# Performance work log

Hardware: AMD Instinct MI355X
Metric: run time of the kernel (lower is better)

The kernel has to match this reference:

```python
import jax, jax.numpy as jnp
import numpy as np

STATE_MASS = 4.0
EPS = 1e-5
LOW_RANK_SCALE = 0.1  # _LOW_RANK_SCALE_INIT


def _ln(x, g, b):
    mu = jnp.mean(x, axis=-1, keepdims=True)
    var = jnp.var(x, axis=-1, keepdims=True)
    return (x - mu) * jax.lax.rsqrt(var + EPS) * g + b


def _signed_abs_softmax(s, axis=-1):
    s = jnp.nan_to_num(s)
    return jnp.sign(s) * jax.nn.softmax(jnp.abs(s), axis=axis)


def _signed_softmax_state(st):
    st = jnp.nan_to_num(st)
    return jnp.sign(st) * jax.nn.softmax(jnp.abs(st), axis=-1) * STATE_MASS


def _low_rank_scores(dst, src, Ut_w, Ut_b, Us_w, Us_b, w):
    # bilinear low-rank pairwise: score[b,i,j] = sum_r (dst_i Ut)_r * w_r * (src_j Us)_r
    pt = dst @ Ut_w + Ut_b                      # [B,Nd,R]
    ps = src @ Us_w + Us_b                      # [B,Ns,R]
    return jnp.einsum('bir,r,bjr->bij', pt, w * LOW_RANK_SCALE, ps)


def _gather_rows(x, idx):
    # x: [B,N,...], idx: [B,M,K] -> [B,M,K,...] (per-batch gather, no NxM broadcast)
    return jax.vmap(lambda xi, ii: xi[ii])(x, idx)


def setup_inputs() -> dict:
    key = jax.random.key(0)
    ks = jax.random.split(key, 8)
    B, S, D, M, R = 16, 2048, 512, 256, 64
    std = 0.02
    return {
        'token_val': jax.random.normal(ks[0], (B, S, D), jnp.float32),
        'token_state': jax.random.normal(ks[1], (B, S), jnp.float32),
        'init_state': jax.random.normal(ks[2], (M,), jnp.float32) * std,
        'init_val': jax.random.normal(ks[3], (M, D), jnp.float32) * std,
        'rUs_w': jax.random.normal(ks[4], (D, R), jnp.float32) * std,
        'rUs_b': jnp.zeros((R,), jnp.float32),
        'rUt_w': jax.random.normal(ks[5], (D, R), jnp.float32) * std,
        'rUt_b': jnp.zeros((R,), jnp.float32),
        'r_w': jnp.ones((R,), jnp.float32),
        'pUs_w': jax.random.normal(ks[6], (D, R), jnp.float32) * std,
        'pUs_b': jnp.zeros((R,), jnp.float32),
        'pUt_w': jax.random.normal(ks[7], (D, R), jnp.float32) * std,
        'pUt_b': jnp.zeros((R,), jnp.float32),
        'p_w': jnp.ones((R,), jnp.float32),
        'ln_g': jnp.ones((D,), jnp.float32),
        'ln_b': jnp.zeros((D,), jnp.float32),
        'topk': 16,
    }


def reference(token_val, token_state, init_state, init_val,
              rUs_w, rUs_b, rUt_w, rUt_b, r_w,
              pUs_w, pUs_b, pUt_w, pUt_b, p_w,
              ln_g, ln_b, topk):
    B = token_val.shape[0]
    M, D = init_val.shape

    # _MemoryLevel.initialize
    mem_state = _signed_softmax_state(jnp.broadcast_to(init_state, (B, M)))
    mem_val = _ln(jnp.broadcast_to(init_val, (B, M, D)), ln_g, ln_b)

    # ---- SparseTransition (write): route tokens -> slots, top-k sources/slot ----
    scores = _low_rank_scores(mem_val, token_val, rUt_w, rUt_b, rUs_w, rUs_b, r_w)  # [B,M,S]
    _, idx = jax.lax.top_k(jnp.abs(scores), topk)              # [B,M,K]
    sel = jnp.take_along_axis(scores, idx, axis=-1)            # [B,M,K]
    edges = _signed_abs_softmax(sel, axis=-1)                  # signed-abs-softmax over edges
    v_sel = _gather_rows(token_val, idx)                       # [B,M,K,D]
    s_sel = _gather_rows(token_state, idx)                     # [B,M,K]
    mem_val = mem_val + jnp.einsum('bmk,bmkd->bmd', edges, v_sel)   # merge_mode='add'
    mem_state = mem_state + jnp.einsum('bmk,bmk->bm', edges, s_sel)
    mem_state = _signed_softmax_state(mem_state)
    mem_val = _ln(mem_val, ln_g, ln_b)

    # ---- SparsePropagation within slots: state-weighted top-k edges, residual ----
    pscores = _low_rank_scores(mem_val, mem_val, pUt_w, pUt_b, pUs_w, pUs_b, p_w)   # [B,M,M]
    pscores = pscores * mem_state[:, None, :]                  # state_weight_edges
    _, pidx = jax.lax.top_k(jnp.abs(pscores), topk)            # [B,M,K]
    psel = jnp.take_along_axis(pscores, pidx, axis=-1)
    pe = _signed_abs_softmax(psel, axis=-1)
    pv = _gather_rows(mem_val, pidx)                           # [B,M,K,D]
    pst = _gather_rows(mem_state, pidx)                        # [B,M,K]
    mem_val = mem_val + jnp.einsum('bmk,bmkd->bmd', pe, pv)    # residual=True
    mem_state = mem_state + jnp.einsum('bmk,bmk->bm', pe, pst)
    mem_state = _signed_softmax_state(mem_state)
    mem_val = _ln(mem_val, ln_g, ln_b)
    return mem_val
```

## Files before the change

### kernel.cpp

```cpp
#include <hip/hip_runtime.h>
#include <hip/hip_bf16.h>
#include <math.h>

#define BB 16
#define SS 2048
#define DD 512
#define MM 256
#define RR 64
#define KK 16
#define GPAD 68

__device__ __forceinline__ float wave_sum(float v) {
#pragma unroll
  for (int off = 32; off > 0; off >>= 1) v += __shfl_xor(v, off);
  return v;
}

__device__ __forceinline__ float sgnf(float v) {
  return (v > 0.f) ? 1.f : ((v < 0.f) ? -1.f : 0.f);
}

__global__ __launch_bounds__(256) void k_init(
    const float* __restrict__ init_val, const float* __restrict__ ln_g,
    const float* __restrict__ ln_b, const float* __restrict__ rUt_w,
    const float* __restrict__ rUt_b, const float* __restrict__ r_w,
    float* __restrict__ mv0, float* __restrict__ pt0) {
  int m = blockIdx.x, t = threadIdx.x;
  __shared__ float row[DD];
  __shared__ float red[8];
  float x0 = init_val[m * DD + t];
  float x1 = init_val[m * DD + t + 256];
  float s = wave_sum(x0 + x1);
  float sq = wave_sum(x0 * x0 + x1 * x1);
  if ((t & 63) == 0) { red[t >> 6] = s; red[4 + (t >> 6)] = sq; }
  __syncthreads();
  float mean = (red[0] + red[1] + red[2] + red[3]) * (1.0f / DD);
  float var = (red[4] + red[5] + red[6] + red[7]) * (1.0f / DD) - mean * mean;
  float rs = rsqrtf(var + 1e-5f);
  float n0 = (x0 - mean) * rs * ln_g[t] + ln_b[t];
  float n1 = (x1 - mean) * rs * ln_g[t + 256] + ln_b[t + 256];
  mv0[m * DD + t] = n0;
  mv0[m * DD + t + 256] = n1;
  row[t] = n0;
  row[t + 256] = n1;
  __syncthreads();
  if (t < RR) {
    float acc = rUt_b[t];
    for (int d = 0; d < DD; ++d) acc += row[d] * rUt_w[d * RR + t];
    pt0[m * RR + t] = acc * r_w[t] * 0.1f;
  }
}

__global__ __launch_bounds__(256) void k_state_softmax(
    const float* __restrict__ in, float* __restrict__ out) {
  int b = blockIdx.x, t = threadIdx.x;
  __shared__ float red[4];
  float v = in[b * MM + t];
  float a = fabsf(v);
  float mx = a;
#pragma unroll
  for (int off = 32; off > 0; off >>= 1) mx = fmaxf(mx, __shfl_xor(mx, off));
  if ((t & 63) == 0) red[t >> 6] = mx;
  __syncthreads();
  mx = fmaxf(fmaxf(red[0], red[1]), fmaxf(red[2], red[3]));
  __syncthreads();
  float e = expf(a - mx);
  float ssum = wave_sum(e);
  if ((t & 63) == 0) red[t >> 6] = ssum;
  __syncthreads();
  ssum = red[0] + red[1] + red[2] + red[3];
  out[b * MM + t] = sgnf(v) * e / ssum * 4.0f;
}

__global__ __launch_bounds__(256) void k_ps(
    const float* __restrict__ A, const float* __restrict__ W,
    const float* __restrict__ bias, float* __restrict__ C0,
    float* __restrict__ C1) {
  __shared__ float Ast[32][128];
  __shared__ float Ws[32][RR];
  int t = threadIdx.x;
  int lane = t & 63;
  int wv = t >> 6;
  int tx = t & 15;
  int ty = t >> 4;
  int half = blockIdx.x >> 8;
  int row0 = (blockIdx.x & 255) * 128;
  int k0 = half * 256;
  float* C = half ? C1 : C0;
  float4 ra[4];
  float4 rw[2];
#pragma unroll
  for (int i = 0; i < 4; ++i) {
    int r = (i & 1) * 64 + lane;
    int k4 = (i >> 1) * 4 + wv;
    ra[i] = *reinterpret_cast<const float4*>(
        &A[(size_t)(row0 + r) * DD + k0 + k4 * 4]);
  }
#pragma unroll
  for (int i = 0; i < 2; ++i) {
    int slot = i * 256 + t;
    int k = slot >> 4, c4 = slot & 15;
    rw[i] = *reinterpret_cast<const float4*>(&W[(size_t)(k0 + k) * RR + c4 * 4]);
  }
  float acc[8][4] = {};
  for (int c = 0; c < 8; ++c) {
    __syncthreads();
#pragma unroll
    for (int i = 0; i < 4; ++i) {
      int r = (i & 1) * 64 + lane;
      int k4 = (i >> 1) * 4 + wv;
      Ast[k4 * 4 + 0][r] = ra[i].x;
      Ast[k4 * 4 + 1][r] = ra[i].y;
      Ast[k4 * 4 + 2][r] = ra[i].z;
      Ast[k4 * 4 + 3][r] = ra[i].w;
    }
#pragma unroll
    for (int i = 0; i < 2; ++i) {
      int slot = i * 256 + t;
      int k = slot >> 4, c4 = slot & 15;
      *reinterpret_cast<float4*>(&Ws[k][c4 * 4]) = rw[i];
    }
    __syncthreads();
    if (c < 7) {
      int kc = k0 + (c + 1) * 32;
#pragma unroll
      for (int i = 0; i < 4; ++i) {
        int r = (i & 1) * 64 + lane;
        int k4 = (i >> 1) * 4 + wv;
        ra[i] = *reinterpret_cast<const float4*>(
            &A[(size_t)(row0 + r) * DD + kc + k4 * 4]);
      }
#pragma unroll
      for (int i = 0; i < 2; ++i) {
        int slot = i * 256 + t;
        int k = slot >> 4, c4 = slot & 15;
        rw[i] = *reinterpret_cast<const float4*>(
            &W[(size_t)(kc + k) * RR + c4 * 4]);
      }
    }
#pragma unroll
    for (int k = 0; k < 32; ++k) {
      float4 alo = *reinterpret_cast<const float4*>(&Ast[k][ty * 8]);
      float4 ahi = *reinterpret_cast<const float4*>(&Ast[k][ty * 8 + 4]);
      float4 w4 = *reinterpret_cast<const float4*>(&Ws[k][tx * 4]);
      acc[0][0] += alo.x * w4.x; acc[0][1] += alo.x * w4.y; acc[0][2] += alo.x * w4.z; acc[0][3] += alo.x * w4.w;
      acc[1][0] += alo.y * w4.x; acc[1][1] += alo.y * w4.y; acc[1][2] += alo.y * w4.z; acc[1][3] += alo.y * w4.w;
      acc[2][0] += alo.z * w4.x; acc[2][1] += alo.z * w4.y; acc[2][2] += alo.z * w4.z; acc[2][3] += alo.z * w4.w;
      acc[3][0] += alo.w * w4.x; acc[3][1] += alo.w * w4.y; acc[3][2] += alo.w * w4.z; acc[3][3] += alo.w * w4.w;
      acc[4][0] += ahi.x * w4.x; acc[4][1] += ahi.x * w4.y; acc[4][2] += ahi.x * w4.z; acc[4][3] += ahi.x * w4.w;
      acc[5][0] += ahi.y * w4.x; acc[5][1] += ahi.y * w4.y; acc[5][2] += ahi.y * w4.z; acc[5][3] += ahi.y * w4.w;
      acc[6][0] += ahi.z * w4.x; acc[6][1] += ahi.z * w4.y; acc[6][2] += ahi.z * w4.z; acc[6][3] += ahi.z * w4.w;
      acc[7][0] += ahi.w * w4.x; acc[7][1] += ahi.w * w4.y; acc[7][2] += ahi.w * w4.z; acc[7][3] += ahi.w * w4.w;
    }
  }
  float4 bv;
  if (half == 0) {
    bv = *reinterpret_cast<const float4*>(&bias[tx * 4]);
  } else {
    bv.x = bv.y = bv.z = bv.w = 0.f;
  }
#pragma unroll
  for (int r = 0; r < 8; ++r) {
    int rr = row0 + ty * 8 + r;
    float4 o;
    o.x = acc[r][0] + bv.x; o.y = acc[r][1] + bv.y;
    o.z = acc[r][2] + bv.z; o.w = acc[r][3] + bv.w;
    *reinterpret_cast<float4*>(&C[(size_t)rr * RR + tx * 4]) = o;
  }
}

template <bool TRANS_OUT>
__device__ __forceinline__ void gemm_body(
    const float* __restrict__ A, const float* __restrict__ W,
    const float* __restrict__ bias, const float* __restrict__ colscale,
    float csmul, const float* __restrict__ rowscale, float* __restrict__ C,
    int row0, float (*Ast)[GPAD], float (*Ws)[GPAD]) {
  int tid = threadIdx.x;
  int ty = tid >> 4, tx = tid & 15;
  float acc[4][4] = {};
  for (int kc = 0; kc < DD; kc += 32) {
#pragma unroll
    for (int i = 0; i < 2; ++i) {
      int s4 = i * 256 + tid;
      int r = s4 >> 3;
      int k4 = s4 & 7;
      float4 v = *reinterpret_cast<const float4*>(
          &A[(size_t)(row0 + r) * DD + kc + k4 * 4]);
      Ast[k4 * 4 + 0][r] = v.x;
      Ast[k4 * 4 + 1][r] = v.y;
      Ast[k4 * 4 + 2][r] = v.z;
      Ast[k4 * 4 + 3][r] = v.w;
    }
#pragma unroll
    for (int i = 0; i < 2; ++i) {
      int s4 = i * 256 + tid;
      int r = s4 >> 4;
      int c4 = s4 & 15;
      float4 v = *reinterpret_cast<const float4*>(
          &W[(size_t)(kc + r) * RR + c4 * 4]);
      *reinterpret_cast<float4*>(&Ws[r][c4 * 4]) = v;
    }
    __syncthreads();
#pragma unroll
    for (int k = 0; k < 32; ++k) {
      float4 a4 = *reinterpret_cast<const float4*>(&Ast[k][ty * 4]);
      float4 w4 = *reinterpret_cast<const float4*>(&Ws[k][tx * 4]);
      acc[0][0] += a4.x * w4.x; acc[0][1] += a4.x * w4.y;
      acc[0][2] += a4.x * w4.z; acc[0][3] += a4.x * w4.w;
      acc[1][0] += a4.y * w4.x; acc[1][1] += a4.y * w4.y;
      acc[1][2] += a4.y * w4.z; acc[1][3] += a4.y * w4.w;
      acc[2][0] += a4.z * w4.x; acc[2][1] += a4.z * w4.y;
      acc[2][2] += a4.z * w4.z; acc[2][3] += a4.z * w4.w;
      acc[3][0] += a4.w * w4.x; acc[3][1] += a4.w * w4.y;
      acc[3][2] += a4.w * w4.z; acc[3][3] += a4.w * w4.w;
    }
    __syncthreads();
  }
#pragma unroll
  for (int i = 0; i < 4; ++i) {
    int rr = row0 + ty * 4 + i;
    float rsc = rowscale ? rowscale[rr] : 1.f;
#pragma unroll
    for (int j = 0; j < 4; ++j) {
      int cc = tx * 4 + j;
      float v = acc[i][j] + bias[cc];
      if (colscale) v *= colscale[cc] * csmul;
      v *= rsc;
      if (TRANS_OUT) {
        C[((size_t)(rr >> 8) * RR + cc) * MM + (rr & 255)] = v;
      } else {
        C[(size_t)rr * RR + cc] = v;
      }
    }
  }
}

__global__ __launch_bounds__(256) void k_gemm_pair(
    const float* __restrict__ mv1, const float* __restrict__ pUt_w,
    const float* __restrict__ pUt_b, const float* __restrict__ p_w,
    const float* __restrict__ pUs_w, const float* __restrict__ pUs_b,
    const float* __restrict__ ms1, float* __restrict__ pt1,
    float* __restrict__ ps1T) {
  __shared__ float Ast[32][GPAD];
  __shared__ float Ws[32][GPAD];
  if (blockIdx.x < 64) {
    gemm_body<false>(mv1, pUt_w, pUt_b, p_w, 0.1f, nullptr, pt1,
                     blockIdx.x * 64, Ast, Ws);
  } else {
    gemm_body<true>(mv1, pUs_w, pUs_b, nullptr, 1.f, ms1, ps1T,
                    (blockIdx.x - 64) * 64, Ast, Ws);
  }
}

#define PSW 144
__device__ __forceinline__ int psw(int j) { return j + ((j >> 5) << 2); }

__global__ __launch_bounds__(256) void k_scores(
    const float* __restrict__ pt0, const float* __restrict__ ps0,
    const float* __restrict__ ps1, float* __restrict__ scores) {
  __shared__ float PtT[RR][64];
  __shared__ float PsT[RR][PSW];
  int t = threadIdx.x;
  int b = blockIdx.z;
  int m0 = blockIdx.y * 64;
  int j0 = blockIdx.x * 128;
  {
    int tm4 = t >> 4, tk4 = t & 15;
    const float* base = pt0 + (size_t)(m0 + tm4 * 4) * RR + tk4 * 4;
    float4 v0 = *reinterpret_cast<const float4*>(base);
    float4 v1 = *reinterpret_cast<const float4*>(base + RR);
    float4 v2 = *reinterpret_cast<const float4*>(base + 2 * RR);
    float4 v3 = *reinterpret_cast<const float4*>(base + 3 * RR);
    float4 w;
    w.x = v0.x; w.y = v1.x; w.z = v2.x; w.w = v3.x;
    *reinterpret_cast<float4*>(&PtT[tk4 * 4 + 0][tm4 * 4]) = w;
    w.x = v0.y; w.y = v1.y; w.z = v2.y; w.w = v3.y;
    *reinterpret_cast<float4*>(&PtT[tk4 * 4 + 1][tm4 * 4]) = w;
    w.x = v0.z; w.y = v1.z; w.z = v2.z; w.w = v3.z;
    *reinterpret_cast<float4*>(&PtT[tk4 * 4 + 2][tm4 * 4]) = w;
    w.x = v0.w; w.y = v1.w; w.z = v2.w; w.w = v3.w;
    *reinterpret_cast<float4*>(&PtT[tk4 * 4 + 3][tm4 * 4]) = w;
  }
#pragma unroll
  for (int ii = 0; ii < 2; ++ii) {
    int slot = ii * 256 + t;
    int jt = slot >> 4, kt = slot & 15;
    size_t off = ((size_t)b * SS + j0 + jt * 4) * RR + kt * 4;
    const float* base0 = ps0 + off;
    const float* base1 = ps1 + off;
    float4 v0 = *reinterpret_cast<const float4*>(base0);
    float4 v1 = *reinterpret_cast<const float4*>(base0 + RR);
    float4 v2 = *reinterpret_cast<const float4*>(base0 + 2 * RR);
    float4 v3 = *reinterpret_cast<const float4*>(base0 + 3 * RR);
    float4 u0 = *reinterpret_cast<const float4*>(base1);
    float4 u1 = *reinterpret_cast<const float4*>(base1 + RR);
    float4 u2 = *reinterpret_cast<const float4*>(base1 + 2 * RR);
    float4 u3 = *reinterpret_cast<const float4*>(base1 + 3 * RR);
    v0.x += u0.x; v0.y += u0.y; v0.z += u0.z; v0.w += u0.w;
    v1.x += u1.x; v1.y += u1.y; v1.z += u1.z; v1.w += u1.w;
    v2.x += u2.x; v2.y += u2.y; v2.z += u2.z; v2.w += u2.w;
    v3.x += u3.x; v3.y += u3.y; v3.z += u3.z; v3.w += u3.w;
    int jc = psw(jt * 4);
    float4 w;
    w.x = v0.x; w.y = v1.x; w.z = v2.x; w.w = v3.x;
    *reinterpret_cast<float4*>(&PsT[kt * 4 + 0][jc]) = w;
    w.x = v0.y; w.y = v1.y; w.z = v2.y; w.w = v3.y;
    *reinterpret_cast<float4*>(&PsT[kt * 4 + 1][jc]) = w;
    w.x = v0.z; w.y = v1.z; w.z = v2.z; w.w = v3.z;
    *reinterpret_cast<float4*>(&PsT[kt * 4 + 2][jc]) = w;
    w.x = v0.w; w.y = v1.w; w.z = v2.w; w.w = v3.w;
    *reinterpret_cast<float4*>(&PsT[kt * 4 + 3][jc]) = w;
  }
  __syncthreads();
  int tj = t & 15;
  int tm = t >> 4;
  int jlo = psw(tj * 8);
  int jhi = psw(tj * 8 + 4);
  float acc[4][8] = {};
#pragma unroll
  for (int k = 0; k < RR; ++k) {
    float4 a4 = *reinterpret_cast<const float4*>(&PtT[k][tm * 4]);
    float4 w0 = *reinterpret_cast<const float4*>(&PsT[k][jlo]);
    float4 w1 = *reinterpret_cast<const float4*>(&PsT[k][jhi]);
    acc[0][0] += a4.x * w0.x; acc[0][1] += a4.x * w0.y; acc[0][2] += a4.x * w0.z; acc[0][3] += a4.x * w0.w;
    acc[0][4] += a4.x * w1.x; acc[0][5] += a4.x * w1.y; acc[0][6] += a4.x * w1.z; acc[0][7] += a4.x * w1.w;
    acc[1][0] += a4.y * w0.x; acc[1][1] += a4.y * w0.y; acc[1][2] += a4.y * w0.z; acc[1][3] += a4.y * w0.w;
    acc[1][4] += a4.y * w1.x; acc[1][5] += a4.y * w1.y; acc[1][6] += a4.y * w1.z; acc[1][7] += a4.y * w1.w;
    acc[2][0] += a4.z * w0.x; acc[2][1] += a4.z * w0.y; acc[2][2] += a4.z * w0.z; acc[2][3] += a4.z * w0.w;
    acc[2][4] += a4.z * w1.x; acc[2][5] += a4.z * w1.y; acc[2][6] += a4.z * w1.z; acc[2][7] += a4.z * w1.w;
    acc[3][0] += a4.w * w0.x; acc[3][1] += a4.w * w0.y; acc[3][2] += a4.w * w0.z; acc[3][3] += a4.w * w0.w;
    acc[3][4] += a4.w * w1.x; acc[3][5] += a4.w * w1.y; acc[3][6] += a4.w * w1.z; acc[3][7] += a4.w * w1.w;
  }
  float* obase = scores + (size_t)b * MM * SS + (size_t)(m0 + tm * 4) * SS + j0 + tj * 8;
#pragma unroll
  for (int i = 0; i < 4; ++i) {
    float4 o0, o1;
    o0.x = acc[i][0]; o0.y = acc[i][1]; o0.z = acc[i][2]; o0.w = acc[i][3];
    o1.x = acc[i][4]; o1.y = acc[i][5]; o1.z = acc[i][6]; o1.w = acc[i][7];
    *reinterpret_cast<float4*>(obase + (size_t)i * SS) = o0;
    *reinterpret_cast<float4*>(obase + (size_t)i * SS + 4) = o1;
  }
}

__global__ __launch_bounds__(256) void k_write(
    const float* __restrict__ scores, const float* __restrict__ token_val,
    const float* __restrict__ token_state, const float* __restrict__ mv0,
    const float* __restrict__ ms0, const float* __restrict__ ln_g,
    const float* __restrict__ ln_b, float* __restrict__ mv1,
    float* __restrict__ ms_w) {
  int t = threadIdx.x;
  int wave = t >> 6, lane = t & 63;
  int i = blockIdx.x;
  int slot = i >> 3;
  int b = 2 * (i & 7) + (slot >> 6);
  int m = (slot & 63) * 4 + wave;
  int row = b * MM + m;
  __shared__ float srl[4][SS];
  __shared__ int selj_sh[4][KK];
  float4* srl4 = reinterpret_cast<float4*>(&srl[wave][0]);
  const float* srow = scores + (size_t)row * SS;
  unsigned maxa = 0u;
#pragma unroll
  for (int ch = 0; ch < 8; ++ch) {
    float4 q = *reinterpret_cast<const float4*>(srow + (ch * 64 + lane) * 4);
    srl4[ch * 64 + lane] = q;
    maxa = max(maxa, __float_as_uint(q.x) & 0x7fffffffu);
    maxa = max(maxa, __float_as_uint(q.y) & 0x7fffffffu);
    maxa = max(maxa, __float_as_uint(q.z) & 0x7fffffffu);
    maxa = max(maxa, __float_as_uint(q.w) & 0x7fffffffu);
  }
#pragma unroll
  for (int off = 32; off > 0; off >>= 1)
    maxa = max(maxa, (unsigned)__shfl_xor((int)maxa, off));
  unsigned lo = 0u, hi = maxa, thr = 0u;
  bool early = false;
  while (lo < hi) {
    unsigned mid = lo + ((hi - lo + 1u) >> 1);
    int cnt = 0;
#pragma unroll
    for (int ch = 0; ch < 8; ++ch) {
      float4 q = srl4[ch * 64 + lane];
      cnt += __popcll(__ballot((__float_as_uint(q.x) & 0x7fffffffu) >= mid));
      cnt += __popcll(__ballot((__float_as_uint(q.y) & 0x7fffffffu) >= mid));
      cnt += __popcll(__ballot((__float_as_uint(q.z) & 0x7fffffffu) >= mid));
      cnt += __popcll(__ballot((__float_as_uint(q.w) & 0x7fffffffu) >= mid));
    }
    if (cnt == KK) { thr = mid; early = true; break; }
    if (cnt > KK) lo = mid; else hi = mid - 1u;
  }
  if (!early) thr = lo;
  unsigned long long ltmask = (1ull << lane) - 1ull;
  int s = 0;
  unsigned tiemask = 0u;
#pragma unroll
  for (int ch = 0; ch < 8; ++ch) {
    float4 q = srl4[ch * 64 + lane];
    unsigned a4[4] = {__float_as_uint(q.x) & 0x7fffffffu,
                      __float_as_uint(q.y) & 0x7fffffffu,
                      __float_as_uint(q.z) & 0x7fffffffu,
                      __float_as_uint(q.w) & 0x7fffffffu};
#pragma unroll
    for (int cc = 0; cc < 4; ++cc) {
      bool sg = early ? (a4[cc] >= thr) : (a4[cc] > thr);
      unsigned long long mk = __ballot(sg);
      if (sg) selj_sh[wave][s + __popcll(mk & ltmask)] = ch * 256 + lane * 4 + cc;
      s += __popcll(mk);
      if (!early && a4[cc] == thr) tiemask |= 1u << (ch * 4 + cc);
    }
  }
  int taken = s;
  while (taken < KK) {
    int myj = 0x7fffffff;
#pragma unroll
    for (int c = 0; c < 32; ++c)
      if ((tiemask >> c) & 1u) {
        int j = (c >> 2) * 256 + lane * 4 + (c & 3);
        myj = min(myj, j);
      }
    int wj = myj;
#pragma unroll
    for (int off = 32; off > 0; off >>= 1) wj = min(wj, __shfl_xor(wj, off));
    if (wj == 0x7fffffff) break;
    if (((wj >> 2) & 63) == lane) tiemask &= ~(1u << (((wj >> 8) << 2) | (wj & 3)));
    if (lane == 0) selj_sh[wave][taken] = wj;
    ++taken;
  }
  int js[KK];
  float es[KK];
#pragma unroll
  for (int k = 0; k < KK; ++k) {
    js[k] = selj_sh[wave][k];
    es[k] = srl[wave][js[k]];
  }
  float mx = 0.f;
#pragma unroll
  for (int k = 0; k < KK; ++k) mx = fmaxf(mx, fabsf(es[k]));
  float ssum = 0.f;
#pragma unroll
  for (int k = 0; k < KK; ++k) {
    float ex = expf(fabsf(es[k]) - mx);
    ssum += ex;
    es[k] = sgnf(es[k]) * ex;
  }
  float inv = 1.f / ssum;
  int dbase = lane * 8;
  const float* m0row = mv0 + m * DD + dbase;
  float4 a0 = *reinterpret_cast<const float4*>(m0row);
  float4 a1 = *reinterpret_cast<const float4*>(m0row + 4);
  float acc[8] = {a0.x, a0.y, a0.z, a0.w, a1.x, a1.y, a1.z, a1.w};
  float stacc = 0.f;
#pragma unroll
  for (int k = 0; k < KK; ++k) {
    float e = es[k] * inv;
    const float* tv = token_val + ((size_t)b * SS + js[k]) * DD + dbase;
    float4 u0 = *reinterpret_cast<const float4*>(tv);
    float4 u1 = *reinterpret_cast<const float4*>(tv + 4);
    acc[0] += e * u0.x; acc[1] += e * u0.y; acc[2] += e * u0.z; acc[3] += e * u0.w;
    acc[4] += e * u1.x; acc[5] += e * u1.y; acc[6] += e * u1.z; acc[7] += e * u1.w;
    stacc += e * token_state[(size_t)b * SS + js[k]];
  }
  if (lane == 0) ms_w[row] = ms0[m] + stacc;
  float s1 = 0.f, s2 = 0.f;
#pragma unroll
  for (int c = 0; c < 8; ++c) { s1 += acc[c]; s2 += acc[c] * acc[c]; }
  s1 = wave_sum(s1);
  s2 = wave_sum(s2);
  float mean = s1 * (1.0f / DD);
  float var = s2 * (1.0f / DD) - mean * mean;
  float rs = rsqrtf(var + 1e-5f);
  float4 g0 = *reinterpret_cast<const float4*>(ln_g + dbase);
  float4 g1 = *reinterpret_cast<const float4*>(ln_g + dbase + 4);
  float4 b0v = *reinterpret_cast<const float4*>(ln_b + dbase);
  float4 b1v = *reinterpret_cast<const float4*>(ln_b + dbase + 4);
  float4 o0, o1;
  o0.x = (acc[0] - mean) * rs * g0.x + b0v.x;
  o0.y = (acc[1] - mean) * rs * g0.y + b0v.y;
  o0.z = (acc[2] - mean) * rs * g0.z + b0v.z;
  o0.w = (acc[3] - mean) * rs * g0.w + b0v.w;
  o1.x = (acc[4] - mean) * rs * g1.x + b1v.x;
  o1.y = (acc[5] - mean) * rs * g1.y + b1v.y;
  o1.z = (acc[6] - mean) * rs * g1.z + b1v.z;
  o1.w = (acc[7] - mean) * rs * g1.w + b1v.w;
  float* orow = mv1 + (size_t)row * DD + dbase;
  *reinterpret_cast<float4*>(orow) = o0;
  *reinterpret_cast<float4*>(orow + 4) = o1;
}

__global__ __launch_bounds__(256, 4) void k_prop(
    const float* __restrict__ pt1, const float* __restrict__ ps1T,
    const float* __restrict__ mv1, const float* __restrict__ ln_g,
    const float* __restrict__ ln_b, float* __restrict__ out) {
  int t = threadIdx.x;
  int wave = t >> 6, lane = t & 63;
  int row = blockIdx.x * 4 + wave;
  int b = row >> 8, m = row & 255;
  __shared__ int selj_sh[4][KK];
  __shared__ float selv_sh[4][KK];
  float ptval = pt1[(size_t)row * RR + lane];
  const float* pB = ps1T + (size_t)b * RR * MM + lane * 4;
  float sc[4] = {0.f, 0.f, 0.f, 0.f};
#pragma unroll 8
  for (int r = 0; r < RR; ++r) {
    float w = __shfl(ptval, r);
    float4 pv = *reinterpret_cast<const float4*>(pB + r * MM);
    sc[0] += w * pv.x; sc[1] += w * pv.y; sc[2] += w * pv.z; sc[3] += w * pv.w;
  }
  int jbase = lane * 4;
  unsigned au[4];
#pragma unroll
  for (int c = 0; c < 4; ++c) au[c] = __float_as_uint(sc[c]) & 0x7fffffffu;
  unsigned lo = 0u, hi = 0x7f800000u, thr = 0u;
  bool early = false;
  while (lo < hi) {
    unsigned mid = lo + ((hi - lo + 1u) >> 1);
    int cnt = 0;
#pragma unroll
    for (int c = 0; c < 4; ++c) cnt += __popcll(__ballot(au[c] >= mid));
    if (cnt == KK) { thr = mid; early = true; break; }
    if (cnt > KK) lo = mid; else hi = mid - 1u;
  }
  if (!early) thr = lo;
  unsigned long long ltmask = (1ull << lane) - 1ull;
  int s = 0;
  unsigned tiemask = 0u;
#pragma unroll
  for (int c = 0; c < 4; ++c) {
    bool sg = early ? (au[c] >= thr) : (au[c] > thr);
    unsigned long long mk = __ballot(sg);
    if (sg) {
      int slot = s + __popcll(mk & ltmask);
      selj_sh[wave][slot] = jbase + c;
      selv_sh[wave][slot] = sc[c];
    }
    s += __popcll(mk);
    if (!early && au[c] == thr) tiemask |= 1u << c;
  }
  int taken = s;
  while (taken < KK) {
    int myj = 0x7fffffff;
#pragma unroll
    for (int c = 0; c < 4; ++c)
      if ((tiemask >> c) & 1u) myj = min(myj, jbase + c);
    int wj = myj;
#pragma unroll
    for (int off = 32; off > 0; off >>= 1) wj = min(wj, __shfl_xor(wj, off));
    if (wj == 0x7fffffff) break;
    if (wj >= jbase && wj < jbase + 4) {
      tiemask &= ~(1u << (wj - jbase));
      selv_sh[wave][taken] = sc[wj - jbase];
      if (lane == (wj >> 2)) selj_sh[wave][taken] = wj;
    }
    ++taken;
  }
  int js[KK];
  float es[KK];
#pragma unroll
  for (int k = 0; k < KK; ++k) { js[k] = selj_sh[wave][k]; es[k] = selv_sh[wave][k]; }
  float mx = 0.f;
#pragma unroll
  for (int k = 0; k < KK; ++k) mx = fmaxf(mx, fabsf(es[k]));
  float ssum = 0.f;
#pragma unroll
  for (int k = 0; k < KK; ++k) {
    float ex = expf(fabsf(es[k]) - mx);
    ssum += ex;
    es[k] = sgnf(es[k]) * ex;
  }
  float inv = 1.f / ssum;
  int dbase = lane * 8;
  const float* mrow = mv1 + (size_t)row * DD + dbase;
  float4 a0 = *reinterpret_cast<const float4*>(mrow);
  float4 a1 = *reinterpret_cast<const float4*>(mrow + 4);
  float acc[8] = {a0.x, a0.y, a0.z, a0.w, a1.x, a1.y, a1.z, a1.w};
#pragma unroll
  for (int k = 0; k < KK; ++k) {
    float e = es[k] * inv;
    const float* pv = mv1 + ((size_t)b * MM + js[k]) * DD + dbase;
    float4 u0 = *reinterpret_cast<const float4*>(pv);
    float4 u1 = *reinterpret_cast<const float4*>(pv + 4);
    acc[0] += e * u0.x; acc[1] += e * u0.y; acc[2] += e * u0.z; acc[3] += e * u0.w;
    acc[4] += e * u1.x; acc[5] += e * u1.y; acc[6] += e * u1.z; acc[7] += e * u1.w;
  }
  float s1 = 0.f, s2 = 0.f;
#pragma unroll
  for (int c = 0; c < 8; ++c) { s1 += acc[c]; s2 += acc[c] * acc[c]; }
  s1 = wave_sum(s1);
  s2 = wave_sum(s2);
  float mean = s1 * (1.0f / DD);
  float var = s2 * (1.0f / DD) - mean * mean;
  float rs = rsqrtf(var + 1e-5f);
  float4 g0 = *reinterpret_cast<const float4*>(ln_g + dbase);
  float4 g1 = *reinterpret_cast<const float4*>(ln_g + dbase + 4);
  float4 b0v = *reinterpret_cast<const float4*>(ln_b + dbase);
  float4 b1v = *reinterpret_cast<const float4*>(ln_b + dbase + 4);
  float4 o0, o1;
  o0.x = (acc[0] - mean) * rs * g0.x + b0v.x;
  o0.y = (acc[1] - mean) * rs * g0.y + b0v.y;
  o0.z = (acc[2] - mean) * rs * g0.z + b0v.z;
  o0.w = (acc[3] - mean) * rs * g0.w + b0v.w;
  o1.x = (acc[4] - mean) * rs * g1.x + b1v.x;
  o1.y = (acc[5] - mean) * rs * g1.y + b1v.y;
  o1.z = (acc[6] - mean) * rs * g1.z + b1v.z;
  o1.w = (acc[7] - mean) * rs * g1.w + b1v.w;
  float* orow = out + (size_t)row * DD + dbase;
  *reinterpret_cast<float4*>(orow) = o0;
  *reinterpret_cast<float4*>(orow + 4) = o1;
}

extern "C" void kernel_launch(void* const* d_in, const int* in_sizes, int n_in,
                              void* d_out, int out_size, void* d_ws,
                              size_t ws_size, hipStream_t stream) {
  const float* token_val = (const float*)d_in[0];
  const float* token_state = (const float*)d_in[1];
  const float* init_state = (const float*)d_in[2];
  const float* init_val = (const float*)d_in[3];
  const float* rUs_w = (const float*)d_in[4];
  const float* rUs_b = (const float*)d_in[5];
  const float* rUt_w = (const float*)d_in[6];
  const float* rUt_b = (const float*)d_in[7];
  const float* r_w = (const float*)d_in[8];
  const float* pUs_w = (const float*)d_in[9];
  const float* pUs_b = (const float*)d_in[10];
  const float* pUt_w = (const float*)d_in[11];
  const float* pUt_b = (const float*)d_in[12];
  const float* p_w = (const float*)d_in[13];
  const float* ln_g = (const float*)d_in[14];
  const float* ln_b = (const float*)d_in[15];
  float* out = (float*)d_out;

  float* ws = (float*)d_ws;
  float* mv0 = ws;    ws += MM * DD;
  float* pt0 = ws;    ws += MM * RR;
  float* ms0 = ws;    ws += MM;
  float* ps = ws;     ws += (size_t)BB * SS * RR;
  float* scores = ws; ws += (size_t)BB * MM * SS;
  float* mv1 = ws;    ws += (size_t)BB * MM * DD;
  float* ms_w = ws;   ws += BB * MM;
  float* ms1 = ws;    ws += BB * MM;
  float* pt1 = ws;    ws += (size_t)BB * MM * RR;
  float* ps1T = ws;   ws += (size_t)BB * RR * MM;
  float* psB = mv1;

  k_init<<<MM, 256, 0, stream>>>(init_val, ln_g, ln_b, rUt_w, rUt_b, r_w, mv0, pt0);
  k_state_softmax<<<1, 256, 0, stream>>>(init_state, ms0);
  k_ps<<<512, 256, 0, stream>>>(token_val, rUs_w, rUs_b, ps, psB);
  dim3 gs(SS / 128, MM / 64, BB);
  k_scores<<<gs, 256, 0, stream>>>(pt0, ps, psB, scores);
  k_write<<<(BB * MM) / 4, 256, 0, stream>>>(scores, token_val, token_state,
                                             mv0, ms0, ln_g, ln_b, mv1, ms_w);
  k_state_softmax<<<BB, 256, 0, stream>>>(ms_w, ms1);
  k_gemm_pair<<<128, 256, 0, stream>>>(mv1, pUt_w, pUt_b, p_w, pUs_w, pUs_b,
                                       ms1, pt1, ps1T);
  k_prop<<<(BB * MM) / 4, 256, 0, stream>>>(pt1, ps1T, mv1, ln_g, ln_b, out);
}
```

Measured before the change: 164.2 us.

## Enlarge register tiles in projection and score GEMMs, cache top-k keys in registers

The token projection kernel now computes 256 rows per block with an 8x8 per-thread register tile, halving the grid. The score kernel now covers 128 slot rows per block with an 8x8 tile, also halving its grid. The top-k kernel keeps the 32 absolute-value keys per lane in registers instead of rereading them from shared memory on every binary-search step. These changes raise arithmetic intensity and cut LDS traffic, at the cost of higher register pressure and fewer blocks, which can reduce occupancy. The projection kernel's global loads also change to one full row per thread, which is less coalesced.

```diff
diff --git a/kernel.cpp b/kernel.cpp
--- a/kernel.cpp
+++ b/kernel.cpp
@@ -76,43 +76,36 @@
     const float* __restrict__ A, const float* __restrict__ W,
     const float* __restrict__ bias, float* __restrict__ C0,
     float* __restrict__ C1) {
-  __shared__ float Ast[32][128];
+  __shared__ float Ast[32][256];
   __shared__ float Ws[32][RR];
   int t = threadIdx.x;
-  int lane = t & 63;
-  int wv = t >> 6;
-  int tx = t & 15;
-  int ty = t >> 4;
-  int half = blockIdx.x >> 8;
-  int row0 = (blockIdx.x & 255) * 128;
+  int cg = t & 7;
+  int rg = t >> 3;
+  int half = blockIdx.x >> 7;
+  int row0 = (blockIdx.x & 127) * 256;
   int k0 = half * 256;
   float* C = half ? C1 : C0;
-  float4 ra[4];
+  float4 ra[8];
   float4 rw[2];
 #pragma unroll
-  for (int i = 0; i < 4; ++i) {
-    int r = (i & 1) * 64 + lane;
-    int k4 = (i >> 1) * 4 + wv;
+  for (int i = 0; i < 8; ++i)
     ra[i] = *reinterpret_cast<const float4*>(
-        &A[(size_t)(row0 + r) * DD + k0 + k4 * 4]);
-  }
+        &A[(size_t)(row0 + t) * DD + k0 + i * 4]);
 #pragma unroll
   for (int i = 0; i < 2; ++i) {
     int slot = i * 256 + t;
     int k = slot >> 4, c4 = slot & 15;
     rw[i] = *reinterpret_cast<const float4*>(&W[(size_t)(k0 + k) * RR + c4 * 4]);
   }
-  float acc[8][4] = {};
+  float acc[8][8] = {};
   for (int c = 0; c < 8; ++c) {
     __syncthreads();
 #pragma unroll
-    for (int i = 0; i < 4; ++i) {
-      int r = (i & 1) * 64 + lane;
-      int k4 = (i >> 1) * 4 + wv;
-      Ast[k4 * 4 + 0][r] = ra[i].x;
-      Ast[k4 * 4 + 1][r] = ra[i].y;
-      Ast[k4 * 4 + 2][r] = ra[i].z;
-      Ast[k4 * 4 + 3][r] = ra[i].w;
+    for (int i = 0; i < 8; ++i) {
+      Ast[i * 4 + 0][t] = ra[i].x;
+      Ast[i * 4 + 1][t] = ra[i].y;
+      Ast[i * 4 + 2][t] = ra[i].z;
+      Ast[i * 4 + 3][t] = ra[i].w;
     }
 #pragma unroll
     for (int i = 0; i < 2; ++i) {
@@ -124,12 +117,9 @@
     if (c < 7) {
       int kc = k0 + (c + 1) * 32;
 #pragma unroll
-      for (int i = 0; i < 4; ++i) {
-        int r = (i & 1) * 64 + lane;
-        int k4 = (i >> 1) * 4 + wv;
+      for (int i = 0; i < 8; ++i)
         ra[i] = *reinterpret_cast<const float4*>(
-            &A[(size_t)(row0 + r) * DD + kc + k4 * 4]);
-      }
+            &A[(size_t)(row0 + t) * DD + kc + i * 4]);
 #pragma unroll
       for (int i = 0; i < 2; ++i) {
         int slot = i * 256 + t;
@@ -140,32 +130,31 @@
     }
 #pragma unroll
     for (int k = 0; k < 32; ++k) {
-      float4 alo = *reinterpret_cast<const float4*>(&Ast[k][ty * 8]);
-      float4 ahi = *reinterpret_cast<const float4*>(&Ast[k][ty * 8 + 4]);
-      float4 w4 = *reinterpret_cast<const float4*>(&Ws[k][tx * 4]);
-      acc[0][0] += alo.x * w4.x; acc[0][1] += alo.x * w4.y; acc[0][2] += alo.x * w4.z; acc[0][3] += alo.x * w4.w;
-      acc[1][0] += alo.y * w4.x; acc[1][1] += alo.y * w4.y; acc[1][2] += alo.y * w4.z; acc[1][3] += alo.y * w4.w;
-      acc[2][0] += alo.z * w4.x; acc[2][1] += alo.z * w4.y; acc[2][2] += alo.z * w4.z; acc[2][3] += alo.z * w4.w;
-      acc[3][0] += alo.w * w4.x; acc[3][1] += alo.w * w4.y; acc[3][2] += alo.w * w4.z; acc[3][3] += alo.w * w4.w;
-      acc[4][0] += ahi.x * w4.x; acc[4][1] += ahi.x * w4.y; acc[4][2] += ahi.x * w4.z; acc[4][3] += ahi.x * w4.w;
-      acc[5][0] += ahi.y * w4.x; acc[5][1] += ahi.y * w4.y; acc[5][2] += ahi.y * w4.z; acc[5][3] += ahi.y * w4.w;
-      acc[6][0] += ahi.z * w4.x; acc[6][1] += ahi.z * w4.y; acc[6][2] += ahi.z * w4.z; acc[6][3] += ahi.z * w4.w;
-      acc[7][0] += ahi.w * w4.x; acc[7][1] += ahi.w * w4.y; acc[7][2] += ahi.w * w4.z; acc[7][3] += ahi.w * w4.w;
-    }
-  }
-  float4 bv;
-  if (half == 0) {
-    bv = *reinterpret_cast<const float4*>(&bias[tx * 4]);
-  } else {
-    bv.x = bv.y = bv.z = bv.w = 0.f;
-  }
+      float4 a0 = *reinterpret_cast<const float4*>(&Ast[k][rg * 8]);
+      float4 a1 = *reinterpret_cast<const float4*>(&Ast[k][rg * 8 + 4]);
+      float4 w0 = *reinterpret_cast<const float4*>(&Ws[k][cg * 8]);
+      float4 w1 = *reinterpret_cast<const float4*>(&Ws[k][cg * 8 + 4]);
+      float av[8] = {a0.x, a0.y, a0.z, a0.w, a1.x, a1.y, a1.z, a1.w};
+      float wv[8] = {w0.x, w0.y, w0.z, w0.w, w1.x, w1.y, w1.z, w1.w};
+#pragma unroll
+      for (int r = 0; r < 8; ++r)
+#pragma unroll
+        for (int cc = 0; cc < 8; ++cc) acc[r][cc] += av[r] * wv[cc];
+    }
+  }
+  float bvx[8];
+#pragma unroll
+  for (int cc = 0; cc < 8; ++cc) bvx[cc] = (half == 0) ? bias[cg * 8 + cc] : 0.f;
 #pragma unroll
   for (int r = 0; r < 8; ++r) {
-    int rr = row0 + ty * 8 + r;
-    float4 o;
-    o.x = acc[r][0] + bv.x; o.y = acc[r][1] + bv.y;
-    o.z = acc[r][2] + bv.z; o.w = acc[r][3] + bv.w;
-    *reinterpret_cast<float4*>(&C[(size_t)rr * RR + tx * 4]) = o;
+    int rr = row0 + rg * 8 + r;
+    float4 o0, o1;
+    o0.x = acc[r][0] + bvx[0]; o0.y = acc[r][1] + bvx[1];
+    o0.z = acc[r][2] + bvx[2]; o0.w = acc[r][3] + bvx[3];
+    o1.x = acc[r][4] + bvx[4]; o1.y = acc[r][5] + bvx[5];
+    o1.z = acc[r][6] + bvx[6]; o1.w = acc[r][7] + bvx[7];
+    *reinterpret_cast<float4*>(&C[(size_t)rr * RR + cg * 8]) = o0;
+    *reinterpret_cast<float4*>(&C[(size_t)rr * RR + cg * 8 + 4]) = o1;
   }
 }
 
@@ -258,14 +247,16 @@
 __global__ __launch_bounds__(256) void k_scores(
     const float* __restrict__ pt0, const float* __restrict__ ps0,
     const float* __restrict__ ps1, float* __restrict__ scores) {
-  __shared__ float PtT[RR][64];
+  __shared__ float PtT[RR][128];
   __shared__ float PsT[RR][PSW];
   int t = threadIdx.x;
   int b = blockIdx.z;
-  int m0 = blockIdx.y * 64;
+  int m0 = blockIdx.y * 128;
   int j0 = blockIdx.x * 128;
-  {
-    int tm4 = t >> 4, tk4 = t & 15;
+#pragma unroll
+  for (int ii = 0; ii < 2; ++ii) {
+    int slot = ii * 256 + t;
+    int tm4 = slot >> 4, tk4 = slot & 15;
     const float* base = pt0 + (size_t)(m0 + tm4 * 4) * RR + tk4 * 4;
     float4 v0 = *reinterpret_cast<const float4*>(base);
     float4 v1 = *reinterpret_cast<const float4*>(base + RR);
@@ -312,33 +303,32 @@
     *reinterpret_cast<float4*>(&PsT[kt * 4 + 3][jc]) = w;
   }
   __syncthreads();
-  int tj = t & 15;
-  int tm = t >> 4;
-  int jlo = psw(tj * 8);
-  int jhi = psw(tj * 8 + 4);
-  float acc[4][8] = {};
+  int jg = t & 15;
+  int mg = t >> 4;
+  int jlo = psw(jg * 8);
+  float acc[8][8] = {};
 #pragma unroll
   for (int k = 0; k < RR; ++k) {
-    float4 a4 = *reinterpret_cast<const float4*>(&PtT[k][tm * 4]);
+    float4 a0 = *reinterpret_cast<const float4*>(&PtT[k][mg * 8]);
+    float4 a1 = *reinterpret_cast<const float4*>(&PtT[k][mg * 8 + 4]);
     float4 w0 = *reinterpret_cast<const float4*>(&PsT[k][jlo]);
-    float4 w1 = *reinterpret_cast<const float4*>(&PsT[k][jhi]);
-    acc[0][0] += a4.x * w0.x; acc[0][1] += a4.x * w0.y; acc[0][2] += a4.x * w0.z; acc[0][3] += a4.x * w0.w;
-    acc[0][4] += a4.x * w1.x; acc[0][5] += a4.x * w1.y; acc[0][6] += a4.x * w1.z; acc[0][7] += a4.x * w1.w;
-    acc[1][0] += a4.y * w0.x; acc[1][1] += a4.y * w0.y; acc[1][2] += a4.y * w0.z; acc[1][3] += a4.y * w0.w;
-    acc[1][4] += a4.y * w1.x; acc[1][5] += a4.y * w1.y; acc[1][6] += a4.y * w1.z; acc[1][7] += a4.y * w1.w;
-    acc[2][0] += a4.z * w0.x; acc[2][1] += a4.z * w0.y; acc[2][2] += a4.z * w0.z; acc[2][3] += a4.z * w0.w;
-    acc[2][4] += a4.z * w1.x; acc[2][5] += a4.z * w1.y; acc[2][6] += a4.z * w1.z; acc[2][7] += a4.z * w1.w;
-    acc[3][0] += a4.w * w0.x; acc[3][1] += a4.w * w0.y; acc[3][2] += a4.w * w0.z; acc[3][3] += a4.w * w0.w;
-    acc[3][4] += a4.w * w1.x; acc[3][5] += a4.w * w1.y; acc[3][6] += a4.w * w1.z; acc[3][7] += a4.w * w1.w;
-  }
-  float* obase = scores + (size_t)b * MM * SS + (size_t)(m0 + tm * 4) * SS + j0 + tj * 8;
-#pragma unroll
-  for (int i = 0; i < 4; ++i) {
+    float4 w1 = *reinterpret_cast<const float4*>(&PsT[k][jlo + 4]);
+    float av[8] = {a0.x, a0.y, a0.z, a0.w, a1.x, a1.y, a1.z, a1.w};
+    float wv[8] = {w0.x, w0.y, w0.z, w0.w, w1.x, w1.y, w1.z, w1.w};
+#pragma unroll
+    for (int r = 0; r < 8; ++r)
+#pragma unroll
+      for (int cc = 0; cc < 8; ++cc) acc[r][cc] += av[r] * wv[cc];
+  }
+  float* obase =
+      scores + (size_t)b * MM * SS + (size_t)(m0 + mg * 8) * SS + j0 + jg * 8;
+#pragma unroll
+  for (int r = 0; r < 8; ++r) {
     float4 o0, o1;
-    o0.x = acc[i][0]; o0.y = acc[i][1]; o0.z = acc[i][2]; o0.w = acc[i][3];
-    o1.x = acc[i][4]; o1.y = acc[i][5]; o1.z = acc[i][6]; o1.w = acc[i][7];
-    *reinterpret_cast<float4*>(obase + (size_t)i * SS) = o0;
-    *reinterpret_cast<float4*>(obase + (size_t)i * SS + 4) = o1;
+    o0.x = acc[r][0]; o0.y = acc[r][1]; o0.z = acc[r][2]; o0.w = acc[r][3];
+    o1.x = acc[r][4]; o1.y = acc[r][5]; o1.z = acc[r][6]; o1.w = acc[r][7];
+    *reinterpret_cast<float4*>(obase + (size_t)r * SS) = o0;
+    *reinterpret_cast<float4*>(obase + (size_t)r * SS + 4) = o1;
   }
 }
 
@@ -359,15 +349,18 @@
   __shared__ int selj_sh[4][KK];
   float4* srl4 = reinterpret_cast<float4*>(&srl[wave][0]);
   const float* srow = scores + (size_t)row * SS;
+  unsigned au[32];
   unsigned maxa = 0u;
 #pragma unroll
   for (int ch = 0; ch < 8; ++ch) {
     float4 q = *reinterpret_cast<const float4*>(srow + (ch * 64 + lane) * 4);
     srl4[ch * 64 + lane] = q;
-    maxa = max(maxa, __float_as_uint(q.x) & 0x7fffffffu);
-    maxa = max(maxa, __float_as_uint(q.y) & 0x7fffffffu);
-    maxa = max(maxa, __float_as_uint(q.z) & 0x7fffffffu);
-    maxa = max(maxa, __float_as_uint(q.w) & 0x7fffffffu);
+    au[ch * 4 + 0] = __float_as_uint(q.x) & 0x7fffffffu;
+    au[ch * 4 + 1] = __float_as_uint(q.y) & 0x7fffffffu;
+    au[ch * 4 + 2] = __float_as_uint(q.z) & 0x7fffffffu;
+    au[ch * 4 + 3] = __float_as_uint(q.w) & 0x7fffffffu;
+    maxa = max(maxa, max(max(au[ch * 4], au[ch * 4 + 1]),
+                         max(au[ch * 4 + 2], au[ch * 4 + 3])));
   }
 #pragma unroll
   for (int off = 32; off > 0; off >>= 1)
@@ -378,13 +371,7 @@
     unsigned mid = lo + ((hi - lo + 1u) >> 1);
     int cnt = 0;
 #pragma unroll
-    for (int ch = 0; ch < 8; ++ch) {
-      float4 q = srl4[ch * 64 + lane];
-      cnt += __popcll(__ballot((__float_as_uint(q.x) & 0x7fffffffu) >= mid));
-      cnt += __popcll(__ballot((__float_as_uint(q.y) & 0x7fffffffu) >= mid));
-      cnt += __popcll(__ballot((__float_as_uint(q.z) & 0x7fffffffu) >= mid));
-      cnt += __popcll(__ballot((__float_as_uint(q.w) & 0x7fffffffu) >= mid));
-    }
+    for (int c = 0; c < 32; ++c) cnt += __popcll(__ballot(au[c] >= mid));
     if (cnt == KK) { thr = mid; early = true; break; }
     if (cnt > KK) lo = mid; else hi = mid - 1u;
   }
@@ -393,20 +380,14 @@
   int s = 0;
   unsigned tiemask = 0u;
 #pragma unroll
-  for (int ch = 0; ch < 8; ++ch) {
-    float4 q = srl4[ch * 64 + lane];
-    unsigned a4[4] = {__float_as_uint(q.x) & 0x7fffffffu,
-                      __float_as_uint(q.y) & 0x7fffffffu,
-                      __float_as_uint(q.z) & 0x7fffffffu,
-                      __float_as_uint(q.w) & 0x7fffffffu};
-#pragma unroll
-    for (int cc = 0; cc < 4; ++cc) {
-      bool sg = early ? (a4[cc] >= thr) : (a4[cc] > thr);
-      unsigned long long mk = __ballot(sg);
-      if (sg) selj_sh[wave][s + __popcll(mk & ltmask)] = ch * 256 + lane * 4 + cc;
-      s += __popcll(mk);
-      if (!early && a4[cc] == thr) tiemask |= 1u << (ch * 4 + cc);
-    }
+  for (int c = 0; c < 32; ++c) {
+    bool sg = early ? (au[c] >= thr) : (au[c] > thr);
+    unsigned long long mk = __ballot(sg);
+    if (sg)
+      selj_sh[wave][s + __popcll(mk & ltmask)] =
+          (c >> 2) * 256 + lane * 4 + (c & 3);
+    s += __popcll(mk);
+    if (!early && au[c] == thr) tiemask |= 1u << c;
   }
   int taken = s;
   while (taken < KK) {
@@ -643,8 +624,8 @@
 
   k_init<<<MM, 256, 0, stream>>>(init_val, ln_g, ln_b, rUt_w, rUt_b, r_w, mv0, pt0);
   k_state_softmax<<<1, 256, 0, stream>>>(init_state, ms0);
-  k_ps<<<512, 256, 0, stream>>>(token_val, rUs_w, rUs_b, ps, psB);
-  dim3 gs(SS / 128, MM / 64, BB);
+  k_ps<<<256, 256, 0, stream>>>(token_val, rUs_w, rUs_b, ps, psB);
+  dim3 gs(SS / 128, MM / 128, BB);
   k_scores<<<gs, 256, 0, stream>>>(pt0, ps, psB, scores);
   k_write<<<(BB * MM) / 4, 256, 0, stream>>>(scores, token_val, token_state,
                                              mv0, ms0, ln_g, ln_b, mv1, ms_w);
```

Result: slower. 172.9 us (+5.3%).
